# Kernel tuning notes

Measured on AMD Instinct MI355X. Metric: run time of the kernel, lower is better.

## Reference

```python
import jax, jax.numpy as jnp
import numpy as np

EPS = 1e-16

def _householder_cascade(vectors):
    # vectors: [N, S, 1]
    v = vectors[..., 0]                                  # [N, S]
    outer = jnp.einsum('ns,nt->nst', v, v)               # [N, S, S]
    inner = jnp.sum(v * v, axis=-1)[:, None, None]       # [N, 1, 1]
    S = v.shape[-1]
    I = jnp.eye(S, dtype=vectors.dtype)
    hh = I[None] - 2.0 * outer / (inner + EPS)           # [N, S, S]
    # sequential left-to-right product: Q = H_0 @ H_1 @ ... @ H_{N-1}
    def step(Q, M):
        return Q @ M, None
    Q, _ = jax.lax.scan(step, I, hh)
    return Q

def setup_inputs() -> dict:
    key = jax.random.key(0)
    k1, k2 = jax.random.split(key)
    S, N, B = 256, 258, 65536
    vectors = jax.random.normal(k1, (N, S, 1), dtype=jnp.float32)
    vectors = vectors / jnp.linalg.norm(vectors, axis=1, keepdims=True)
    x = jax.random.normal(k2, (B, S), dtype=jnp.float32)
    return {"x": x, "vectors": vectors}

def reference(x, vectors):
    Q = _householder_cascade(vectors)   # [S, S]
    return x @ Q.T
```

## Files before the change

### kernel.cpp

```cpp
#include <hip/hip_runtime.h>


#define GLOAD_LDS16(g, l)                                                      \
  __builtin_amdgcn_global_load_lds(                                            \
      (const __attribute__((address_space(1))) void*)(g),                      \
      (__attribute__((address_space(3))) void*)(l), 16, 0, 0)

typedef __attribute__((ext_vector_type(8))) short bf16x8;
typedef __attribute__((ext_vector_type(4))) float f32x4;

__device__ __forceinline__ unsigned short f2bf_rne(float f) {
  unsigned u = __builtin_bit_cast(unsigned, f);
  return (unsigned short)((u + 0x7fffu + ((u >> 16) & 1u)) >> 16);
}

template <int CTRL>
__device__ __forceinline__ float dpp_add(float v) {
  int t = __builtin_amdgcn_update_dpp(0, __builtin_bit_cast(int, v), CTRL, 0xF,
                                      0xF, true);
  return v + __builtin_bit_cast(float, t);
}

__global__ void hh_scale(const float* __restrict__ vecs, float* __restrict__ u) {
  const int n = blockIdx.x;
  const int l = threadIdx.x;
  float4* uo = (float4*)(u + (long)n * 256) + l;
  if (n >= 258) {
    *uo = make_float4(0.f, 0.f, 0.f, 0.f);
    return;
  }
  const float4 v = *((const float4*)(vecs + (long)n * 256) + l);
  float p = v.x * v.x + v.y * v.y + v.z * v.z + v.w * v.w;
#pragma unroll
  for (int off = 32; off; off >>= 1) p += __shfl_xor(p, off);
  const float s = sqrtf(2.0f / (p + 1e-16f));
  *uo = make_float4(v.x * s, v.y * s, v.z * s, v.w * s);
}

__launch_bounds__(64, 1)
__global__ void hh_qchunk(const float* __restrict__ u,
                          float* __restrict__ Qc) {
  const int l = threadIdx.x;
  const int chunk = blockIdx.x >> 6;
  const int rg = blockIdx.x & 63;
  const int r = l >> 4;
  const int c = l & 15;
  const int row = rg * 4 + r;
  const int col0 = c * 16;

  float q[16];
#pragma unroll
  for (int i = 0; i < 16; ++i) q[i] = (col0 + i == row) ? 1.f : 0.f;

  const float* ub = u + (long)chunk * 33 * 256 + col0;

  auto load16 = [&](float(&d)[16], int n) {
    const float4* v = (const float4*)(ub + (long)n * 256);
#pragma unroll
    for (int i = 0; i < 4; ++i) {
      float4 t = v[i];
      d[4 * i] = t.x; d[4 * i + 1] = t.y; d[4 * i + 2] = t.z; d[4 * i + 3] = t.w;
    }
  };

  auto step = [&](const float(&a)[16]) {
    float p0 = 0.f, p1 = 0.f, p2 = 0.f, p3 = 0.f;
#pragma unroll
    for (int e = 0; e < 4; ++e) {
      p0 = fmaf(q[e], a[e], p0);
      p1 = fmaf(q[4 + e], a[4 + e], p1);
      p2 = fmaf(q[8 + e], a[8 + e], p2);
      p3 = fmaf(q[12 + e], a[12 + e], p3);
    }
    float p = (p0 + p1) + (p2 + p3);
    p = dpp_add<0xB1>(p);
    p = dpp_add<0x4E>(p);
    p = dpp_add<0x124>(p);
    p = dpp_add<0x128>(p);
#pragma unroll
    for (int k = 0; k < 16; ++k) q[k] = fmaf(-p, a[k], q[k]);
  };

  float A0[16], A1[16];
  load16(A0, 0);
  load16(A1, 1);
  for (int n = 0; n < 32; n += 2) {
    step(A0);
    load16(A0, n + 2);
    step(A1);
    load16(A1, n + 3);
  }
  step(A0);

  float4* out = (float4*)(Qc + (long)chunk * 65536 + row * 256 + col0);
#pragma unroll
  for (int i = 0; i < 4; ++i)
    out[i] = make_float4(q[4 * i], q[4 * i + 1], q[4 * i + 2], q[4 * i + 3]);
}

__launch_bounds__(256)
__global__ void hh_mm(const float* __restrict__ in, float* __restrict__ out,
                      unsigned short* __restrict__ outb, int to_bf16) {
  const int b = blockIdx.x >> 6;
  const int t = blockIdx.x & 63;
  const int ti = (t >> 3) * 32, tj = (t & 7) * 32;
  const int tid = threadIdx.x;
  const int tx = tid & 15, ty = tid >> 4;
  const float* A = in + (long)b * 2 * 65536;
  const float* Bm = A + 65536;

  __shared__ float As[32][68];
  __shared__ float Bs[64][36];

  float acc00 = 0.f, acc01 = 0.f, acc10 = 0.f, acc11 = 0.f;

  for (int k0 = 0; k0 < 256; k0 += 64) {
#pragma unroll
    for (int u0 = 0; u0 < 2048; u0 += 1024) {
      int idx = u0 + tid * 4;
      int rr = idx >> 6, cc = idx & 63;
      *(float4*)&As[rr][cc] = *(const float4*)&A[(ti + rr) * 256 + k0 + cc];
      int kk = idx >> 5, jj = idx & 31;
      *(float4*)&Bs[kk][jj] = *(const float4*)&Bm[(k0 + kk) * 256 + tj + jj];
    }
    __syncthreads();
#pragma unroll 8
    for (int kk = 0; kk < 64; ++kk) {
      float a0 = As[2 * ty][kk], a1 = As[2 * ty + 1][kk];
      float b0 = Bs[kk][2 * tx], b1 = Bs[kk][2 * tx + 1];
      acc00 = fmaf(a0, b0, acc00);
      acc01 = fmaf(a0, b1, acc01);
      acc10 = fmaf(a1, b0, acc10);
      acc11 = fmaf(a1, b1, acc11);
    }
    __syncthreads();
  }

  const int gi = ti + 2 * ty, gj = tj + 2 * tx;
  if (to_bf16) {
    unsigned short* o = outb + (long)b * 65536;
    o[gi * 256 + gj] = f2bf_rne(acc00);
    o[gi * 256 + gj + 1] = f2bf_rne(acc01);
    o[(gi + 1) * 256 + gj] = f2bf_rne(acc10);
    o[(gi + 1) * 256 + gj + 1] = f2bf_rne(acc11);
  } else {
    float* o = out + (long)b * 65536;
    o[gi * 256 + gj] = acc00;
    o[gi * 256 + gj + 1] = acc01;
    o[(gi + 1) * 256 + gj] = acc10;
    o[(gi + 1) * 256 + gj + 1] = acc11;
  }
}

__launch_bounds__(512)
__global__ void hh_gemm(const float* __restrict__ X,
                        const unsigned short* __restrict__ Qb,
                        float* __restrict__ Y) {
  __shared__ __align__(128) char lds[65536];
  const int tid = threadIdx.x;
  const int lane = tid & 63;
  const int wid = tid >> 6;
  const int wm = wid >> 2;
  const int wn = wid & 3;
  const int fr = lane & 15;
  const int fg = lane >> 4;
  const long bm0 = (long)blockIdx.x * 128;

  auto stage = [&](int buf, int kt) {
#pragma unroll
    for (int r2 = 0; r2 < 2; ++r2) {
      int slot = r2 * 512 + tid;
      int row = slot >> 3, seg = slot & 7;
      int ps = seg ^ (row & 7);
      GLOAD_LDS16(X + (bm0 + row) * 256 + kt * 32 + ps * 4,
                  lds + buf * 16384 + slot * 16);
    }
#pragma unroll
    for (int r2 = 0; r2 < 2; ++r2) {
      int slot = r2 * 512 + tid;
      int row = slot >> 2, seg = slot & 3;
      int ps = seg ^ (row & 3);
      GLOAD_LDS16(Qb + row * 256 + kt * 32 + ps * 8,
                  lds + 32768 + buf * 16384 + slot * 16);
    }
  };

  f32x4 acc[4][4];
#pragma unroll
  for (int m = 0; m < 4; ++m)
#pragma unroll
    for (int n = 0; n < 4; ++n) acc[m][n] = (f32x4){0.f, 0.f, 0.f, 0.f};

  stage(0, 0);
  __syncthreads();

  for (int kt = 0; kt < 8; ++kt) {
    const int cur = kt & 1;
    if (kt < 7) stage(cur ^ 1, kt + 1);

    bf16x8 aF[4], bF[4];
#pragma unroll
    for (int m = 0; m < 4; ++m) {
      int row = wm * 64 + m * 16 + fr;
      int s0 = (2 * fg) ^ (row & 7);
      int s1 = (2 * fg + 1) ^ (row & 7);
      const f32x4 x0 = *(const f32x4*)(lds + cur * 16384 + row * 128 + s0 * 16);
      const f32x4 x1 = *(const f32x4*)(lds + cur * 16384 + row * 128 + s1 * 16);
      bf16x8 t;
      t[0] = (short)f2bf_rne(x0[0]);
      t[1] = (short)f2bf_rne(x0[1]);
      t[2] = (short)f2bf_rne(x0[2]);
      t[3] = (short)f2bf_rne(x0[3]);
      t[4] = (short)f2bf_rne(x1[0]);
      t[5] = (short)f2bf_rne(x1[1]);
      t[6] = (short)f2bf_rne(x1[2]);
      t[7] = (short)f2bf_rne(x1[3]);
      aF[m] = t;
    }
#pragma unroll
    for (int n = 0; n < 4; ++n) {
      int row = wn * 64 + n * 16 + fr;
      int ps = fg ^ (row & 3);
      bF[n] = *(const bf16x8*)(lds + 32768 + cur * 16384 + row * 64 + ps * 16);
    }
#pragma unroll
    for (int m = 0; m < 4; ++m)
#pragma unroll
      for (int n = 0; n < 4; ++n)
        acc[m][n] =
            __builtin_amdgcn_mfma_f32_16x16x32_bf16(aF[m], bF[n], acc[m][n], 0, 0, 0);
    __syncthreads();
  }

#pragma unroll
  for (int m = 0; m < 4; ++m)
#pragma unroll
    for (int n = 0; n < 4; ++n)
#pragma unroll
      for (int r = 0; r < 4; ++r) {
        long grow = bm0 + wm * 64 + m * 16 + fg * 4 + r;
        int gcol = wn * 64 + n * 16 + fr;
        Y[grow * 256 + gcol] = acc[m][n][r];
      }
}

extern "C" void kernel_launch(void* const* d_in, const int* in_sizes, int n_in,
                              void* d_out, int out_size, void* d_ws, size_t ws_size,
                              hipStream_t stream) {
  const float* x = (const float*)d_in[0];
  const float* vecs = (const float*)d_in[1];
  float* y = (float*)d_out;

  char* ws = (char*)d_ws;
  float* u = (float*)ws;
  unsigned short* Qb = (unsigned short*)(ws + 278528);

  char* ob = (char*)d_out;
  float* Qc = (float*)(ob);
  float* P = (float*)(ob + 2097152);
  float* R = (float*)(ob + 3145728);

  hh_scale<<<272, 64, 0, stream>>>(vecs, u);
  hh_qchunk<<<512, 64, 0, stream>>>(u, Qc);
  hh_mm<<<256, 256, 0, stream>>>(Qc, P, nullptr, 0);
  hh_mm<<<128, 256, 0, stream>>>(P, R, nullptr, 0);
  hh_mm<<<64, 256, 0, stream>>>(R, nullptr, Qb, 1);
  hh_gemm<<<512, 512, 0, stream>>>(x, Qb, y);
}
```

Measured before the change: 65.81 us.

## Use split-bf16 MFMA for the Householder chunk-merge matrix products

Replaces the scalar FP32 LDS-tiled matmul used to merge the partial Householder products with a kernel that splits each fp32 operand into a hi and lo bf16 pair. It runs three bf16 MFMAs per tile (hi*hi, hi*lo, lo*hi) to approximate fp32 accuracy on the matrix cores. Tiles grow to 64x64 per block, so far fewer blocks are launched (64/32/16). Operands are read straight from global memory without LDS, and the B operand is read with strided per-element loads, which may hurt memory efficiency. The split-bf16 scheme also gives slightly lower precision than true fp32.

Measured after the change: 75.66 us. 15.0% more time.

```diff
diff --git a/kernel.cpp b/kernel.cpp
--- a/kernel.cpp
+++ b/kernel.cpp
@@ -12,6 +12,17 @@
 __device__ __forceinline__ unsigned short f2bf_rne(float f) {
   unsigned u = __builtin_bit_cast(unsigned, f);
   return (unsigned short)((u + 0x7fffu + ((u >> 16) & 1u)) >> 16);
+}
+
+struct bfpair { short hi, lo; };
+
+__device__ __forceinline__ bfpair bf_split(float x) {
+  unsigned short hu = f2bf_rne(x);
+  float hf = __builtin_bit_cast(float, (unsigned)hu << 16);
+  bfpair r;
+  r.hi = (short)hu;
+  r.lo = (short)f2bf_rne(x - hf);
+  return r;
 }
 
 template <int CTRL>
@@ -99,57 +110,78 @@
 }
 
 __launch_bounds__(256)
-__global__ void hh_mm(const float* __restrict__ in, float* __restrict__ out,
-                      unsigned short* __restrict__ outb, int to_bf16) {
-  const int b = blockIdx.x >> 6;
-  const int t = blockIdx.x & 63;
-  const int ti = (t >> 3) * 32, tj = (t & 7) * 32;
+__global__ void hh_merge(const float* __restrict__ in, float* __restrict__ out,
+                         unsigned short* __restrict__ outb, int to_bf16) {
+  const int b = blockIdx.x >> 4;
+  const int t = blockIdx.x & 15;
+  const int bi = (t >> 2) * 64, bj = (t & 3) * 64;
   const int tid = threadIdx.x;
-  const int tx = tid & 15, ty = tid >> 4;
+  const int lane = tid & 63, wid = tid >> 6;
+  const int wm = wid >> 1, wn = wid & 1;
+  const int fr = lane & 15, fg = lane >> 4;
   const float* A = in + (long)b * 2 * 65536;
   const float* Bm = A + 65536;
 
-  __shared__ float As[32][68];
-  __shared__ float Bs[64][36];
-
-  float acc00 = 0.f, acc01 = 0.f, acc10 = 0.f, acc11 = 0.f;
-
-  for (int k0 = 0; k0 < 256; k0 += 64) {
-#pragma unroll
-    for (int u0 = 0; u0 < 2048; u0 += 1024) {
-      int idx = u0 + tid * 4;
-      int rr = idx >> 6, cc = idx & 63;
-      *(float4*)&As[rr][cc] = *(const float4*)&A[(ti + rr) * 256 + k0 + cc];
-      int kk = idx >> 5, jj = idx & 31;
-      *(float4*)&Bs[kk][jj] = *(const float4*)&Bm[(k0 + kk) * 256 + tj + jj];
-    }
-    __syncthreads();
-#pragma unroll 8
-    for (int kk = 0; kk < 64; ++kk) {
-      float a0 = As[2 * ty][kk], a1 = As[2 * ty + 1][kk];
-      float b0 = Bs[kk][2 * tx], b1 = Bs[kk][2 * tx + 1];
-      acc00 = fmaf(a0, b0, acc00);
-      acc01 = fmaf(a0, b1, acc01);
-      acc10 = fmaf(a1, b0, acc10);
-      acc11 = fmaf(a1, b1, acc11);
-    }
-    __syncthreads();
+  const int ar0 = bi + wm * 32;
+  const int bc0 = bj + wn * 32;
+
+  f32x4 acc[2][2];
+#pragma unroll
+  for (int m = 0; m < 2; ++m)
+#pragma unroll
+    for (int n = 0; n < 2; ++n) acc[m][n] = (f32x4){0.f, 0.f, 0.f, 0.f};
+
+  for (int kt = 0; kt < 8; ++kt) {
+    const int k0 = kt * 32 + fg * 8;
+    bf16x8 ahi[2], alo[2], bhi[2], blo[2];
+#pragma unroll
+    for (int m = 0; m < 2; ++m) {
+      const float* ap = A + (long)(ar0 + m * 16 + fr) * 256 + k0;
+      f32x4 x0 = *(const f32x4*)ap;
+      f32x4 x1 = *(const f32x4*)(ap + 4);
+#pragma unroll
+      for (int e = 0; e < 4; ++e) {
+        bfpair p0 = bf_split(x0[e]);
+        bfpair p1 = bf_split(x1[e]);
+        ahi[m][e] = p0.hi; alo[m][e] = p0.lo;
+        ahi[m][4 + e] = p1.hi; alo[m][4 + e] = p1.lo;
+      }
+    }
+#pragma unroll
+    for (int n = 0; n < 2; ++n) {
+      const float* bp = Bm + (long)k0 * 256 + bc0 + n * 16 + fr;
+#pragma unroll
+      for (int e = 0; e < 8; ++e) {
+        bfpair pb = bf_split(bp[e * 256]);
+        bhi[n][e] = pb.hi; blo[n][e] = pb.lo;
+      }
+    }
+#pragma unroll
+    for (int m = 0; m < 2; ++m)
+#pragma unroll
+      for (int n = 0; n < 2; ++n) {
+        acc[m][n] = __builtin_amdgcn_mfma_f32_16x16x32_bf16(ahi[m], bhi[n],
+                                                            acc[m][n], 0, 0, 0);
+        acc[m][n] = __builtin_amdgcn_mfma_f32_16x16x32_bf16(ahi[m], blo[n],
+                                                            acc[m][n], 0, 0, 0);
+        acc[m][n] = __builtin_amdgcn_mfma_f32_16x16x32_bf16(alo[m], bhi[n],
+                                                            acc[m][n], 0, 0, 0);
+      }
   }
 
-  const int gi = ti + 2 * ty, gj = tj + 2 * tx;
-  if (to_bf16) {
-    unsigned short* o = outb + (long)b * 65536;
-    o[gi * 256 + gj] = f2bf_rne(acc00);
-    o[gi * 256 + gj + 1] = f2bf_rne(acc01);
-    o[(gi + 1) * 256 + gj] = f2bf_rne(acc10);
-    o[(gi + 1) * 256 + gj + 1] = f2bf_rne(acc11);
-  } else {
-    float* o = out + (long)b * 65536;
-    o[gi * 256 + gj] = acc00;
-    o[gi * 256 + gj + 1] = acc01;
-    o[(gi + 1) * 256 + gj] = acc10;
-    o[(gi + 1) * 256 + gj + 1] = acc11;
-  }
+#pragma unroll
+  for (int m = 0; m < 2; ++m)
+#pragma unroll
+    for (int n = 0; n < 2; ++n)
+#pragma unroll
+      for (int rr = 0; rr < 4; ++rr) {
+        const int grow = ar0 + m * 16 + fg * 4 + rr;
+        const int gcol = bc0 + n * 16 + fr;
+        if (to_bf16)
+          outb[(long)b * 65536 + grow * 256 + gcol] = f2bf_rne(acc[m][n][rr]);
+        else
+          out[(long)b * 65536 + grow * 256 + gcol] = acc[m][n][rr];
+      }
 }
 
 __launch_bounds__(512)
@@ -262,8 +294,8 @@
 
   hh_scale<<<272, 64, 0, stream>>>(vecs, u);
   hh_qchunk<<<512, 64, 0, stream>>>(u, Qc);
-  hh_mm<<<256, 256, 0, stream>>>(Qc, P, nullptr, 0);
-  hh_mm<<<128, 256, 0, stream>>>(P, R, nullptr, 0);
-  hh_mm<<<64, 256, 0, stream>>>(R, nullptr, Qb, 1);
+  hh_merge<<<64, 256, 0, stream>>>(Qc, P, nullptr, 0);
+  hh_merge<<<32, 256, 0, stream>>>(P, R, nullptr, 0);
+  hh_merge<<<16, 256, 0, stream>>>(R, nullptr, Qb, 1);
   hh_gemm<<<512, 512, 0, stream>>>(x, Qb, y);
 }
```
